# Kernel tuning notes

Hardware: AMD Instinct MI355X
Metric: run time of the kernel (lower is better)

Reference implementation:

```python
import jax, jax.numpy as jnp
from jax import lax
import numpy as np

B, CIN, COUT, WDIM, SIN, K = 8, 512, 512, 512, 64, 3
UP, DOWN, TAPS = 2, 2, 12
PX0, PX1, PY0, PY1 = 9, 8, 9, 8  # from StyleGAN3 padding formula for these rates
CLAMP, SLOPE = 256.0, 0.2
GAIN = float(np.sqrt(2.0))
FS_TMP, CUTOFF, HALFW = 128.0, 16.0, 16.0
DN = ('NCHW', 'OIHW', 'NCHW')


def _kaiser_beta(a):
    if a > 50.0:
        return 0.1102 * (a - 8.7)
    if a > 21.0:
        return 0.5842 * (a - 21.0) ** 0.4 + 0.07886 * (a - 21.0)
    return 0.0


def _firwin(numtaps, cutoff, width, fs):
    # replicates scipy.signal.firwin(numtaps, cutoff, width=width, fs=fs)
    nyq = fs / 2.0
    atten = 2.285 * (numtaps - 1) * np.pi * (width / nyq) + 7.95
    beta = _kaiser_beta(atten)
    win = np.kaiser(numtaps, beta)
    m = np.arange(numtaps) - (numtaps - 1) / 2.0
    fc = cutoff / nyq
    h = fc * np.sinc(fc * m) * win
    h /= h.sum()
    return h.astype(np.float32)


def setup_inputs() -> dict:
    key = jax.random.key(0)
    ks = jax.random.split(key, 4)
    f = jnp.asarray(_firwin(TAPS, CUTOFF, 2.0 * HALFW, FS_TMP))
    return {
        'x': jax.random.normal(ks[0], (B, CIN, SIN, SIN), jnp.float32),
        'w': jax.random.normal(ks[1], (B, WDIM), jnp.float32),
        'affine_w': jax.random.normal(ks[2], (CIN, WDIM), jnp.float32),
        'affine_b': jnp.ones((CIN,), jnp.float32),  # bias_init=1
        'conv_w': jax.random.normal(ks[3], (COUT, CIN, K, K), jnp.float32),
        'conv_b': jnp.zeros((COUT,), jnp.float32),
        'up_filter': f,
        'down_filter': f,  # same cutoff/width/fs for in and out here
    }


def _depthwise(x, f1d, axis, stride=1, pad=(0, 0), lhs_dil=1):
    # separable depthwise FIR along one spatial axis (axis 2 = H, 3 = W)
    C, t = x.shape[1], f1d.shape[0]
    if axis == 2:
        k = jnp.broadcast_to(f1d.reshape(1, 1, t, 1), (C, 1, t, 1))
        return lax.conv_general_dilated(x, k, (stride, 1), [pad, (0, 0)],
                                        lhs_dilation=(lhs_dil, 1),
                                        feature_group_count=C, dimension_numbers=DN)
    k = jnp.broadcast_to(f1d.reshape(1, 1, 1, t), (C, 1, 1, t))
    return lax.conv_general_dilated(x, k, (1, stride), [(0, 0), pad],
                                    lhs_dilation=(1, lhs_dil),
                                    feature_group_count=C, dimension_numbers=DN)


def reference(x, w, affine_w, affine_b, conv_w, conv_b, up_filter, down_filter):
    # --- affine: FullyConnectedLayer(w_dim, in_channels, bias_init=1) ---
    styles = w @ (affine_w.T * (1.0 / np.sqrt(WDIM))) + affine_b  # [B, CIN]
    # --- modulated_conv2d with demodulation (input_gain = ema.rsqrt() = 1) ---
    wt = conv_w * lax.rsqrt(jnp.mean(conv_w ** 2, axis=(1, 2, 3), keepdims=True))
    s = styles * lax.rsqrt(jnp.mean(styles ** 2))
    ww = wt[None] * s[:, None, :, None, None]                     # [B,COUT,CIN,K,K]
    ww = ww * lax.rsqrt(jnp.sum(ww ** 2, axis=(2, 3, 4)) + 1e-8)[:, :, None, None, None]
    conv1 = lambda xi, wi: lax.conv_general_dilated(
        xi[None], wi, (1, 1), [(K - 1, K - 1)] * 2, dimension_numbers=DN)[0]
    x = jax.vmap(conv1)(x, ww)                                    # [B,COUT,66,66]
    # --- filtered_lrelu: bias -> upfirdn(up) -> lrelu*gain, clamp -> upfirdn(down) ---
    x = x + conv_b[None, :, None, None]
    fu = up_filter[::-1] * UP  # flip_filter=False; per-pass gain = up (total up^2)
    x = _depthwise(x, fu, 2, pad=(PY0, PY1 + UP - 1), lhs_dil=UP)
    x = _depthwise(x, fu, 3, pad=(PX0, PX1 + UP - 1), lhs_dil=UP)  # [B,COUT,138,138]
    x = jnp.clip(jnp.where(x >= 0, x, SLOPE * x) * GAIN, -CLAMP, CLAMP)
    fd = down_filter[::-1]
    x = _depthwise(x, fd, 2, stride=DOWN)
    x = _depthwise(x, fd, 3, stride=DOWN)                          # [B,COUT,64,64]
    return x
```

## Files before the change

### kernel.cpp

```cpp
#include <hip/hip_runtime.h>

typedef __attribute__((ext_vector_type(4))) float floatx4;
typedef __attribute__((ext_vector_type(8))) short short8;

#define AS1(p) ((const __attribute__((address_space(1))) unsigned int*)(p))
#define AS3(p) ((__attribute__((address_space(3))) unsigned int*)(p))

static __device__ __forceinline__ void async16(const void* g, void* l) {
  __builtin_amdgcn_global_load_lds(AS1(g), AS3(l), 16, 0, 0);
}

static __device__ __forceinline__ unsigned short f2bf(float f) {
  unsigned u = __float_as_uint(f);
  unsigned r = u + 0x7FFFu + ((u >> 16) & 1u);
  return (unsigned short)(r >> 16);
}
static __device__ __forceinline__ unsigned packbf(float lo, float hi) {
  unsigned ul = __float_as_uint(lo), uh = __float_as_uint(hi);
  ul = ul + 0x7FFFu + ((ul >> 16) & 1u);
  uh = uh + 0x7FFFu + ((uh >> 16) & 1u);
  return (ul >> 16) | (uh & 0xFFFF0000u);
}
static __device__ __forceinline__ float bf2f(unsigned short h) {
  return __uint_as_float(((unsigned)h) << 16);
}
static __device__ __forceinline__ float bf_lo(unsigned u) { return __uint_as_float(u << 16); }
static __device__ __forceinline__ float bf_hi(unsigned u) { return __uint_as_float(u & 0xFFFF0000u); }

__global__ void k_styles(const float* __restrict__ w, const float* __restrict__ aw,
                         const float* __restrict__ ab, float* __restrict__ styles) {
  int t = blockIdx.x * 256 + threadIdx.x;
  int b = t >> 9, c = t & 511;
  float acc = 0.f;
  for (int d = 0; d < 512; ++d) acc += w[b * 512 + d] * aw[c * 512 + d];
  styles[t] = acc * 0.04419417382415922f + ab[c];
}

__global__ void k_msr(const float* __restrict__ styles, float* __restrict__ msr) {
  __shared__ float red[256];
  float acc = 0.f;
  for (int i = threadIdx.x; i < 4096; i += 256) { float v = styles[i]; acc += v * v; }
  red[threadIdx.x] = acc; __syncthreads();
  for (int s = 128; s > 0; s >>= 1) {
    if ((int)threadIdx.x < s) red[threadIdx.x] += red[threadIdx.x + s];
    __syncthreads();
  }
  if (threadIdx.x == 0) *msr = rsqrtf(red[0] / 4096.0f);
}

__global__ void k_wstat(const float* __restrict__ cw, float* __restrict__ t, float* __restrict__ q) {
  int o = blockIdx.x, tid = threadIdx.x;
  __shared__ float red[256];
  float tot = 0.f;
  for (int i = tid; i < 512; i += 256) {
    const float* p = cw + ((size_t)o * 512 + i) * 9;
    float s = 0.f;
#pragma unroll
    for (int k = 0; k < 9; ++k) s += p[k] * p[k];
    q[o * 512 + i] = s;
    tot += s;
  }
  red[tid] = tot; __syncthreads();
  for (int s2 = 128; s2 > 0; s2 >>= 1) {
    if (tid < s2) red[tid] += red[tid + s2];
    __syncthreads();
  }
  if (tid == 0) t[o] = rsqrtf(red[0] / 4608.0f);
}

__global__ void k_dmod(const float* __restrict__ styles, const float* __restrict__ msr,
                       const float* __restrict__ t, const float* __restrict__ q,
                       float* __restrict__ g) {
  int idx = blockIdx.x * 256 + threadIdx.x;
  int b = idx >> 9, o = idx & 511;
  float m = *msr;
  float acc = 0.f;
  for (int i = 0; i < 512; ++i) {
    float s = styles[b * 512 + i] * m;
    acc += s * s * q[o * 512 + i];
  }
  float to = t[o];
  g[idx] = to * rsqrtf(to * to * acc + 1e-8f);
}

__global__ __launch_bounds__(256) void k_wpack(const float* __restrict__ cw,
                                               const float* __restrict__ styles,
                                               const float* __restrict__ msr,
                                               const float* __restrict__ g,
                                               unsigned short* __restrict__ wbf2) {
  __shared__ float raw[512][11];
  int o = blockIdx.x, tid = threadIdx.x;
  for (int i = tid; i < 512; i += 256) {
    const float* p = cw + ((size_t)o * 512 + i) * 9;
#pragma unroll
    for (int k = 0; k < 9; ++k) raw[i][k] = p[k];
  }
  __syncthreads();
  float m = *msr;
  const int nb = o >> 7, wn = (o >> 6) & 1, ni = (o >> 4) & 3, ol = o & 15;
  for (int b = 0; b < 8; ++b) {
    float gg = g[b * 512 + o];
    const size_t base_bo = ((size_t)(b * 4 + nb) * 2 + wn);
    for (int f = tid; f < 9 * 512; f += 256) {
      int s = f >> 9, i = f & 511;
      int ic = i >> 5, qq = (i >> 3) & 3, j = i & 7;
      float v = raw[i][s] * gg * (styles[b * 512 + i] * m);
      size_t idx = ((((base_bo * 9 + s) * 16 + ic) * 4 + ni) * 512) + (qq * 16 + ol) * 8 + j;
      wbf2[idx] = f2bf(v);
    }
  }
}

__global__ __launch_bounds__(256) void k_xpack(const float* __restrict__ x,
                                               unsigned short* __restrict__ xp) {
  __shared__ float tile[64][65];
  int Y = blockIdx.x, cc0 = blockIdx.y * 64, b = blockIdx.z;
  int tid = threadIdx.x;
  int yy = Y - 2;
  bool valid = (yy >= 0 && yy < 64);
  if (valid) {
    for (int it = 0; it < 16; ++it) {
      int f = it * 256 + tid;
      int cc = f >> 6, xx = f & 63;
      tile[xx][cc] = x[(((size_t)b * 512 + cc0 + cc) * 64 + yy) * 64 + xx];
    }
  }
  __syncthreads();
  for (int it = 0; it < 17; ++it) {
    int f = it * 256 + tid;
    int X = f >> 6, cc = f & 63;
    int xx = X - 2;
    float v = (valid && xx >= 0 && xx < 64) ? tile[xx][cc] : 0.f;
    xp[(((size_t)b * 68 + Y) * 68 + X) * 512 + cc0 + cc] = f2bf(v);
  }
}

__global__ __launch_bounds__(256, 2) void k_conv(const unsigned short* __restrict__ xp,
                                                 const unsigned short* __restrict__ wbf2,
                                                 const float* __restrict__ cb,
                                                 float* __restrict__ y) {
  __shared__ __align__(16) unsigned short lds[24576];
  const int tid = threadIdx.x;
  const int w = tid >> 6, lane = tid & 63;
  const int wm = w & 1, wn = w >> 1;
  const int q = lane >> 4, ln = lane & 15;

  const int xcd = blockIdx.x & 7;
  const int slot = blockIdx.x >> 3;
  const int combo = xcd * 4 + slot / 35;
  const int mt = slot % 35;
  const int nt = combo & 3;
  const int b = combo >> 2;
  const int m0 = mt * 128, n0 = nt * 128;
  const int oy0 = m0 / 66;

  const unsigned short* xpb = xp + (size_t)b * (68 * 68 * 512);

  size_t gof_p[6];
#pragma unroll
  for (int i = 0; i < 6; ++i) {
    int pv = w * 96 + i * 16 + (lane >> 2);
    int pve = pv < 339 ? pv : 339;
    int r = pve / 68, px = pve - r * 68;
    int Y = oy0 + r; if (Y > 67) Y = 67;
    int ch = ((lane & 3) ^ ((pve >> 1) & 3)) * 8;
    gof_p[i] = (size_t)(Y * 68 + px) * 512 + ch;
  }

  int pvA[4];
#pragma unroll
  for (int mi = 0; mi < 4; ++mi) {
    int p = m0 + wm * 64 + mi * 16 + ln; if (p > 4355) p = 4355;
    int oy = p / 66, ox = p - oy * 66;
    pvA[mi] = (oy - oy0) * 68 + ox;
  }

  const unsigned short* wB = wbf2 + (((size_t)(b * 4 + nt) * 2 + wn) * 294912) + (size_t)lane * 8;

  floatx4 acc[4][4];
#pragma unroll
  for (int i = 0; i < 4; ++i)
#pragma unroll
    for (int j = 0; j < 4; ++j) acc[i][j] = (floatx4){0.f, 0.f, 0.f, 0.f};

  unsigned short* pat0 = lds;
  unsigned short* pat1 = lds + 12288;

#pragma unroll
  for (int i = 0; i < 6; ++i)
    async16(xpb + gof_p[i], pat0 + (w * 96 + i * 16) * 32);

  short8 bF[4];
#pragma unroll
  for (int ni = 0; ni < 4; ++ni)
    bF[ni] = *(const short8*)(wB + ni * 512);

  for (int ic = 0; ic < 16; ++ic) {
    asm volatile("s_waitcnt vmcnt(0)" ::: "memory");
    asm volatile("s_barrier" ::: "memory");
    const unsigned short* pb = (ic & 1) ? pat1 : pat0;
    unsigned short* pn = (ic & 1) ? pat0 : pat1;
    const size_t pchan = (size_t)(ic + 1) * 32;
#pragma unroll
    for (int s = 0; s < 9; ++s) {
      if (s >= 1 && s <= 6 && ic < 15)
        async16(xpb + gof_p[s - 1] + pchan, pn + (w * 96 + (s - 1) * 16) * 32);
      const int sn = (s < 8) ? s + 1 : 0;
      const int icn = (s < 8) ? ic : (ic < 15 ? ic + 1 : 15);
      const unsigned short* wBn = wB + ((size_t)sn * 16 + icn) * 2048;
      short8 bN[4];
#pragma unroll
      for (int ni = 0; ni < 4; ++ni) bN[ni] = *(const short8*)(wBn + ni * 512);
      const int d = (s / 3) * 68 + (s % 3);
      short8 aF[4];
#pragma unroll
      for (int mi = 0; mi < 4; ++mi) {
        int pv = pvA[mi] + d;
        int off = pv * 32 + ((q ^ ((pv >> 1) & 3)) << 3);
        aF[mi] = *(const short8*)(pb + off);
      }
#pragma unroll
      for (int mi = 0; mi < 4; ++mi)
#pragma unroll
        for (int ni = 0; ni < 4; ++ni)
          acc[mi][ni] = __builtin_amdgcn_mfma_f32_16x16x32_bf16(aF[mi], bF[ni], acc[mi][ni], 0, 0, 0);
#pragma unroll
      for (int ni = 0; ni < 4; ++ni) bF[ni] = bN[ni];
    }
  }

  __syncthreads();
  float* slab = (float*)lds + w * 2176;
  const int pbase = m0 + wm * 64;
  const bool pok = (pbase + ln * 4) < 4356;
  float cbv[4];
#pragma unroll
  for (int ni = 0; ni < 4; ++ni) cbv[ni] = cb[n0 + wn * 64 + ni * 16 + ln];

#pragma unroll
  for (int pass = 0; pass < 2; ++pass) {
#pragma unroll
    for (int ni2 = 0; ni2 < 2; ++ni2) {
      const int ni = pass * 2 + ni2;
#pragma unroll
      for (int mi = 0; mi < 4; ++mi) {
        float4 v;
        v.x = acc[mi][ni][0] + cbv[ni];
        v.y = acc[mi][ni][1] + cbv[ni];
        v.z = acc[mi][ni][2] + cbv[ni];
        v.w = acc[mi][ni][3] + cbv[ni];
        *(float4*)&slab[(ni2 * 16 + ln) * 68 + mi * 16 + q * 4] = v;
      }
    }
#pragma unroll
    for (int i = 0; i < 8; ++i) {
      const int orow = i * 4 + q;
      const int o = n0 + wn * 64 + pass * 32 + orow;
      if (pok) {
        float4 vv = *(const float4*)&slab[orow * 68 + ln * 4];
        *(float4*)&y[((size_t)b * 512 + o) * 4356 + pbase + ln * 4] = vv;
      }
    }
  }
}

__global__ __launch_bounds__(256, 4) void k_updown(const float* __restrict__ yg,
                                                   const float* __restrict__ uf,
                                                   const float* __restrict__ df,
                                                   float* __restrict__ out) {
  __shared__ __align__(16) unsigned short zraw[138 * 88];
  __shared__ __align__(16) unsigned short t1buf[138 * 56];
  const int tid = threadIdx.x;
  const int plane = blockIdx.x >> 1;
  const int s = blockIdx.x & 1;
  const float* yp = yg + (size_t)plane * 4356;

  float fub[12], fuc[12], fdw[12];
#pragma unroll
  for (int i = 0; i < 12; ++i) {
    float u = uf[11 - i] * 2.0f;
    fub[i] = u;
    fuc[i] = u * 1.41421356237309515f;
    fdw[i] = df[11 - i];
  }

  float* ybuf = (float*)zraw;
  const int xoff = 32 * s - 4;
  for (int t = tid; t < 75 * 48; t += 256) {
    int row = t / 48, col = t - row * 48;
    int r = row - 4, x = xoff + col;
    float v = (r >= 0 && r < 66 && x >= 0 && x < 66) ? yp[r * 66 + x] : 0.f;
    ybuf[t] = v;
  }
  __syncthreads();

  for (int t = tid; t < 69 * 6; t += 256) {
    int v = t / 6, c = t - v * 6;
    float ae[8], ao[8];
#pragma unroll
    for (int e = 0; e < 8; ++e) { ae[e] = 0.f; ao[e] = 0.f; }
#pragma unroll
    for (int u = 0; u < 6; ++u) {
      const float* yr = &ybuf[(v + u) * 48 + 8 * c];
      float4 p0 = *(const float4*)yr;
      float4 p1 = *(const float4*)(yr + 4);
      float fe = fub[2 * u + 1], fo = fub[2 * u];
      ae[0] += p0.x * fe; ao[0] += p0.x * fo;
      ae[1] += p0.y * fe; ao[1] += p0.y * fo;
      ae[2] += p0.z * fe; ao[2] += p0.z * fo;
      ae[3] += p0.w * fe; ao[3] += p0.w * fo;
      ae[4] += p1.x * fe; ao[4] += p1.x * fo;
      ae[5] += p1.y * fe; ao[5] += p1.y * fo;
      ae[6] += p1.z * fe; ao[6] += p1.z * fo;
      ae[7] += p1.w * fe; ao[7] += p1.w * fo;
    }
    uint4 se, so;
    se.x = packbf(ae[0], ae[1]); se.y = packbf(ae[2], ae[3]);
    se.z = packbf(ae[4], ae[5]); se.w = packbf(ae[6], ae[7]);
    so.x = packbf(ao[0], ao[1]); so.y = packbf(ao[2], ao[3]);
    so.z = packbf(ao[4], ao[5]); so.w = packbf(ao[6], ao[7]);
    *(uint4*)&t1buf[(2 * v) * 56 + 8 * c] = se;
    *(uint4*)&t1buf[(2 * v + 1) * 56 + 8 * c] = so;
  }
  __syncthreads();

  for (int t = tid; t < 138 * 5; t += 256) {
    int Y = t / 5, k = t - Y * 5;
    const unsigned short* tr = &t1buf[Y * 56 + 8 * k];
    uint4 r0 = *(const uint4*)tr;
    uint4 r1 = *(const uint4*)(tr + 8);
    float a[14];
    a[0] = bf_lo(r0.x);  a[1] = bf_hi(r0.x);
    a[2] = bf_lo(r0.y);  a[3] = bf_hi(r0.y);
    a[4] = bf_lo(r0.z);  a[5] = bf_hi(r0.z);
    a[6] = bf_lo(r0.w);  a[7] = bf_hi(r0.w);
    a[8] = bf_lo(r1.x);  a[9] = bf_hi(r1.x);
    a[10] = bf_lo(r1.y); a[11] = bf_hi(r1.y);
    a[12] = bf_lo(r1.z); a[13] = bf_hi(r1.z);
    float ae[8], ao[8];
#pragma unroll
    for (int p = 0; p < 8; ++p) { ae[p] = 0.f; ao[p] = 0.f; }
#pragma unroll
    for (int u = 0; u < 6; ++u) {
      float fe = fuc[2 * u + 1], fo = fuc[2 * u];
#pragma unroll
      for (int p = 0; p < 8; ++p) {
        float tv = a[p + u];
        ae[p] += tv * fe;
        ao[p] += tv * fo;
      }
    }
    uint4 s0, s1;
    float ze[8], zo[8];
#pragma unroll
    for (int p = 0; p < 8; ++p) {
      float v0 = fmaxf(ae[p], 0.f) + 0.2f * fminf(ae[p], 0.f);
      float v1 = fmaxf(ao[p], 0.f) + 0.2f * fminf(ao[p], 0.f);
      ze[p] = fminf(fmaxf(v0, -256.f), 256.f);
      zo[p] = fminf(fmaxf(v1, -256.f), 256.f);
    }
    s0.x = packbf(ze[0], zo[0]); s0.y = packbf(ze[1], zo[1]);
    s0.z = packbf(ze[2], zo[2]); s0.w = packbf(ze[3], zo[3]);
    s1.x = packbf(ze[4], zo[4]); s1.y = packbf(ze[5], zo[5]);
    s1.z = packbf(ze[6], zo[6]); s1.w = packbf(ze[7], zo[7]);
    unsigned short* zr = &zraw[Y * 88 + 16 * k];
    *(uint4*)zr = s0;
    *(uint4*)(zr + 8) = s1;
  }
  __syncthreads();

  unsigned short* t2 = t1buf;
  for (int t = tid; t < 64 * 10; t += 256) {
    int yr = t / 10, k = t - yr * 10;
    float acc[8];
#pragma unroll
    for (int e = 0; e < 8; ++e) acc[e] = 0.f;
#pragma unroll
    for (int i = 0; i < 12; ++i) {
      uint4 zv = *(const uint4*)&zraw[(2 * yr + i) * 88 + 8 * k];
      float c = fdw[i];
      acc[0] += c * bf_lo(zv.x); acc[1] += c * bf_hi(zv.x);
      acc[2] += c * bf_lo(zv.y); acc[3] += c * bf_hi(zv.y);
      acc[4] += c * bf_lo(zv.z); acc[5] += c * bf_hi(zv.z);
      acc[6] += c * bf_lo(zv.w); acc[7] += c * bf_hi(zv.w);
    }
    uint4 st;
    st.x = packbf(acc[0], acc[1]); st.y = packbf(acc[2], acc[3]);
    st.z = packbf(acc[4], acc[5]); st.w = packbf(acc[6], acc[7]);
    *(uint4*)&t2[yr * 88 + 8 * k] = st;
  }
  __syncthreads();

  {
    int t = tid;
    int yr = t >> 2, ce = t & 3;
    const unsigned short* tr = &t2[yr * 88 + 16 * ce];
    uint4 q0 = *(const uint4*)tr;
    uint4 q1 = *(const uint4*)(tr + 8);
    uint4 q2 = *(const uint4*)(tr + 16);
    uint4 q3 = *(const uint4*)(tr + 24);
    float wv[26];
    wv[0] = bf_lo(q0.x);  wv[1] = bf_hi(q0.x);
    wv[2] = bf_lo(q0.y);  wv[3] = bf_hi(q0.y);
    wv[4] = bf_lo(q0.z);  wv[5] = bf_hi(q0.z);
    wv[6] = bf_lo(q0.w);  wv[7] = bf_hi(q0.w);
    wv[8] = bf_lo(q1.x);  wv[9] = bf_hi(q1.x);
    wv[10] = bf_lo(q1.y); wv[11] = bf_hi(q1.y);
    wv[12] = bf_lo(q1.z); wv[13] = bf_hi(q1.z);
    wv[14] = bf_lo(q1.w); wv[15] = bf_hi(q1.w);
    wv[16] = bf_lo(q2.x); wv[17] = bf_hi(q2.x);
    wv[18] = bf_lo(q2.y); wv[19] = bf_hi(q2.y);
    wv[20] = bf_lo(q2.z); wv[21] = bf_hi(q2.z);
    wv[22] = bf_lo(q2.w); wv[23] = bf_hi(q2.w);
    wv[24] = bf_lo(q3.x); wv[25] = bf_hi(q3.x);
    float ov[8];
#pragma unroll
    for (int e = 0; e < 8; ++e) {
      float acc = 0.f;
#pragma unroll
      for (int j = 0; j < 12; ++j) acc += fdw[j] * wv[2 * e + j];
      ov[e] = acc;
    }
    float* op = out + (size_t)plane * 4096 + yr * 64 + 32 * s + 8 * ce;
    *(float4*)op = (float4){ov[0], ov[1], ov[2], ov[3]};
    *(float4*)(op + 4) = (float4){ov[4], ov[5], ov[6], ov[7]};
  }
}

extern "C" void kernel_launch(void* const* d_in, const int* in_sizes, int n_in,
                              void* d_out, int out_size, void* d_ws, size_t ws_size,
                              hipStream_t stream) {
  const float* x  = (const float*)d_in[0];
  const float* w  = (const float*)d_in[1];
  const float* aw = (const float*)d_in[2];
  const float* ab = (const float*)d_in[3];
  const float* cw = (const float*)d_in[4];
  const float* cb = (const float*)d_in[5];
  const float* uf = (const float*)d_in[6];
  const float* df = (const float*)d_in[7];
  float* out = (float*)d_out;
  char* ws = (char*)d_ws;

  float* styles = (float*)(ws + 0);
  float* msr    = (float*)(ws + 16384);
  float* tbuf   = (float*)(ws + 16640);
  float* qbuf   = (float*)(ws + 18688);
  float* gbuf   = (float*)(ws + 1067264);
  unsigned short* xp   = (unsigned short*)(ws + 1083648);
  unsigned short* wbf2 = (unsigned short*)(ws + 38963456);
  float* yb            = (float*)(ws + 76712192);

  k_styles<<<16, 256, 0, stream>>>(w, aw, ab, styles);
  k_msr<<<1, 256, 0, stream>>>(styles, msr);
  k_wstat<<<512, 256, 0, stream>>>(cw, tbuf, qbuf);
  k_dmod<<<16, 256, 0, stream>>>(styles, msr, tbuf, qbuf, gbuf);
  k_wpack<<<512, 256, 0, stream>>>(cw, styles, msr, gbuf, wbf2);
  k_xpack<<<dim3(68, 8, 8), 256, 0, stream>>>(x, xp);
  k_conv<<<1120, 256, 0, stream>>>(xp, wbf2, cb, yb);
  k_updown<<<8192, 256, 0, stream>>>(yb, uf, df, out);
}
```

Baseline: 539.5 us.

## Halve conv M-tile, raise occupancy, deepen weight prefetch and simplify block mapping

The implicit-GEMM conv kernel's M tile shrinks from 128 to 64 output pixels, and its launch bound rises to 4 blocks per CU. The smaller LDS patch (4 rows padded to 80 columns) and fewer accumulators allow more blocks per CU and more blocks overall. Weight fragments are now prefetched two steps ahead with a partial vmcnt wait instead of a full drain. The XCD-aware block remap is dropped for a plain batch-interleaved mapping, and the output store is reorganised. Each block now reloads a larger halo relative to its work, and the change in L2 locality from the new block mapping is uncertain.

Measured after the change: 555.6 us. 1.03x slower.

```diff
diff --git a/kernel.cpp b/kernel.cpp
--- a/kernel.cpp
+++ b/kernel.cpp
@@ -135,104 +135,104 @@
   }
 }
 
-__global__ __launch_bounds__(256, 2) void k_conv(const unsigned short* __restrict__ xp,
+__global__ __launch_bounds__(256, 4) void k_conv(const unsigned short* __restrict__ xp,
                                                  const unsigned short* __restrict__ wbf2,
                                                  const float* __restrict__ cb,
                                                  float* __restrict__ y) {
-  __shared__ __align__(16) unsigned short lds[24576];
+  __shared__ __align__(16) unsigned short lds[20480];
   const int tid = threadIdx.x;
   const int w = tid >> 6, lane = tid & 63;
   const int wm = w & 1, wn = w >> 1;
   const int q = lane >> 4, ln = lane & 15;
 
-  const int xcd = blockIdx.x & 7;
-  const int slot = blockIdx.x >> 3;
-  const int combo = xcd * 4 + slot / 35;
-  const int mt = slot % 35;
-  const int nt = combo & 3;
-  const int b = combo >> 2;
-  const int m0 = mt * 128, n0 = nt * 128;
+  const int b = blockIdx.x & 7;
+  const int rest = blockIdx.x >> 3;
+  const int nt = rest / 69;
+  const int mt = rest - nt * 69;
+  const int m0 = mt * 64, n0 = nt * 128;
   const int oy0 = m0 / 66;
 
   const unsigned short* xpb = xp + (size_t)b * (68 * 68 * 512);
 
-  size_t gof_p[6];
-#pragma unroll
-  for (int i = 0; i < 6; ++i) {
-    int pv = w * 96 + i * 16 + (lane >> 2);
-    int pve = pv < 339 ? pv : 339;
-    int r = pve / 68, px = pve - r * 68;
-    int Y = oy0 + r; if (Y > 67) Y = 67;
-    int ch = ((lane & 3) ^ ((pve >> 1) & 3)) * 8;
-    gof_p[i] = (size_t)(Y * 68 + px) * 512 + ch;
-  }
-
-  int pvA[4];
-#pragma unroll
-  for (int mi = 0; mi < 4; ++mi) {
-    int p = m0 + wm * 64 + mi * 16 + ln; if (p > 4355) p = 4355;
+  size_t gof_p[5];
+  {
+    int Y = oy0 + w; if (Y > 67) Y = 67;
+#pragma unroll
+    for (int i = 0; i < 5; ++i) {
+      int col = i * 16 + (lane >> 2);
+      int vpad = w * 80 + col;
+      int X = col > 67 ? 67 : col;
+      int csrc = (lane & 3) ^ ((vpad >> 1) & 3);
+      gof_p[i] = (size_t)(Y * 68 + X) * 512 + csrc * 8;
+    }
+  }
+
+  int pvA[2];
+#pragma unroll
+  for (int mi = 0; mi < 2; ++mi) {
+    int p = m0 + wm * 32 + mi * 16 + ln; if (p > 4355) p = 4355;
     int oy = p / 66, ox = p - oy * 66;
-    pvA[mi] = (oy - oy0) * 68 + ox;
+    pvA[mi] = (oy - oy0) * 80 + ox;
   }
 
   const unsigned short* wB = wbf2 + (((size_t)(b * 4 + nt) * 2 + wn) * 294912) + (size_t)lane * 8;
 
-  floatx4 acc[4][4];
-#pragma unroll
-  for (int i = 0; i < 4; ++i)
+  floatx4 acc[2][4];
+#pragma unroll
+  for (int i = 0; i < 2; ++i)
 #pragma unroll
     for (int j = 0; j < 4; ++j) acc[i][j] = (floatx4){0.f, 0.f, 0.f, 0.f};
 
   unsigned short* pat0 = lds;
-  unsigned short* pat1 = lds + 12288;
-
-#pragma unroll
-  for (int i = 0; i < 6; ++i)
-    async16(xpb + gof_p[i], pat0 + (w * 96 + i * 16) * 32);
-
-  short8 bF[4];
-#pragma unroll
-  for (int ni = 0; ni < 4; ++ni)
-    bF[ni] = *(const short8*)(wB + ni * 512);
+  unsigned short* pat1 = lds + 10240;
+
+#pragma unroll
+  for (int i = 0; i < 5; ++i)
+    async16(xpb + gof_p[i], pat0 + (w * 80 + i * 16) * 32);
+
+  short8 bA[4], bB[4];
+#pragma unroll
+  for (int ni = 0; ni < 4; ++ni) bA[ni] = *(const short8*)(wB + ni * 512);
+#pragma unroll
+  for (int ni = 0; ni < 4; ++ni) bB[ni] = *(const short8*)(wB + 16 * 2048 + ni * 512);
 
   for (int ic = 0; ic < 16; ++ic) {
-    asm volatile("s_waitcnt vmcnt(0)" ::: "memory");
+    asm volatile("s_waitcnt vmcnt(8)" ::: "memory");
     asm volatile("s_barrier" ::: "memory");
     const unsigned short* pb = (ic & 1) ? pat1 : pat0;
     unsigned short* pn = (ic & 1) ? pat0 : pat1;
     const size_t pchan = (size_t)(ic + 1) * 32;
+    const int icn = ic < 15 ? ic + 1 : 15;
 #pragma unroll
     for (int s = 0; s < 9; ++s) {
-      if (s >= 1 && s <= 6 && ic < 15)
-        async16(xpb + gof_p[s - 1] + pchan, pn + (w * 96 + (s - 1) * 16) * 32);
-      const int sn = (s < 8) ? s + 1 : 0;
-      const int icn = (s < 8) ? ic : (ic < 15 ? ic + 1 : 15);
-      const unsigned short* wBn = wB + ((size_t)sn * 16 + icn) * 2048;
-      short8 bN[4];
-#pragma unroll
-      for (int ni = 0; ni < 4; ++ni) bN[ni] = *(const short8*)(wBn + ni * 512);
-      const int d = (s / 3) * 68 + (s % 3);
-      short8 aF[4];
-#pragma unroll
-      for (int mi = 0; mi < 4; ++mi) {
+      if (s < 5 && ic < 15)
+        async16(xpb + gof_p[s] + pchan, pn + (w * 80 + s * 16) * 32);
+      const int ss2 = (s <= 6) ? s + 2 : s - 7;
+      const int ic2 = (s <= 6) ? ic : icn;
+      const unsigned short* wBn = wB + ((size_t)(ss2 * 16 + ic2)) * 2048;
+      short8 bC[4];
+#pragma unroll
+      for (int ni = 0; ni < 4; ++ni) bC[ni] = *(const short8*)(wBn + ni * 512);
+      const int d = (s / 3) * 80 + (s % 3);
+      short8 aF[2];
+#pragma unroll
+      for (int mi = 0; mi < 2; ++mi) {
         int pv = pvA[mi] + d;
         int off = pv * 32 + ((q ^ ((pv >> 1) & 3)) << 3);
         aF[mi] = *(const short8*)(pb + off);
       }
 #pragma unroll
-      for (int mi = 0; mi < 4; ++mi)
+      for (int mi = 0; mi < 2; ++mi)
 #pragma unroll
         for (int ni = 0; ni < 4; ++ni)
-          acc[mi][ni] = __builtin_amdgcn_mfma_f32_16x16x32_bf16(aF[mi], bF[ni], acc[mi][ni], 0, 0, 0);
-#pragma unroll
-      for (int ni = 0; ni < 4; ++ni) bF[ni] = bN[ni];
-    }
-  }
-
-  __syncthreads();
-  float* slab = (float*)lds + w * 2176;
-  const int pbase = m0 + wm * 64;
-  const bool pok = (pbase + ln * 4) < 4356;
+          acc[mi][ni] = __builtin_amdgcn_mfma_f32_16x16x32_bf16(aF[mi], bA[ni], acc[mi][ni], 0, 0, 0);
+#pragma unroll
+      for (int ni = 0; ni < 4; ++ni) { bA[ni] = bB[ni]; bB[ni] = bC[ni]; }
+    }
+  }
+
+  float* slab = (float*)lds + w * 1152;
+  const int pbase = m0 + wm * 32;
   float cbv[4];
 #pragma unroll
   for (int ni = 0; ni < 4; ++ni) cbv[ni] = cb[n0 + wn * 64 + ni * 16 + ln];
@@ -243,23 +243,24 @@
     for (int ni2 = 0; ni2 < 2; ++ni2) {
       const int ni = pass * 2 + ni2;
 #pragma unroll
-      for (int mi = 0; mi < 4; ++mi) {
+      for (int mi = 0; mi < 2; ++mi) {
         float4 v;
         v.x = acc[mi][ni][0] + cbv[ni];
         v.y = acc[mi][ni][1] + cbv[ni];
         v.z = acc[mi][ni][2] + cbv[ni];
         v.w = acc[mi][ni][3] + cbv[ni];
-        *(float4*)&slab[(ni2 * 16 + ln) * 68 + mi * 16 + q * 4] = v;
+        *(float4*)&slab[(ni2 * 16 + ln) * 36 + mi * 16 + q * 4] = v;
       }
     }
-#pragma unroll
-    for (int i = 0; i < 8; ++i) {
-      const int orow = i * 4 + q;
-      const int o = n0 + wn * 64 + pass * 32 + orow;
-      if (pok) {
-        float4 vv = *(const float4*)&slab[orow * 68 + ln * 4];
-        *(float4*)&y[((size_t)b * 512 + o) * 4356 + pbase + ln * 4] = vv;
-      }
+    const int ol = lane >> 1;
+    const int ph = (lane & 1) * 16;
+    const int o = n0 + wn * 64 + pass * 32 + ol;
+    float* dst = &y[((size_t)b * 512 + o) * 4356 + pbase + ph];
+#pragma unroll
+    for (int j = 0; j < 4; ++j) {
+      const int p4 = pbase + ph + j * 4;
+      if (p4 < 4356)
+        *(float4*)(dst + j * 4) = *(const float4*)&slab[ol * 36 + ph + j * 4];
     }
   }
 }
@@ -456,6 +457,6 @@
   k_dmod<<<16, 256, 0, stream>>>(styles, msr, tbuf, qbuf, gbuf);
   k_wpack<<<512, 256, 0, stream>>>(cw, styles, msr, gbuf, wbf2);
   k_xpack<<<dim3(68, 8, 8), 256, 0, stream>>>(x, xp);
-  k_conv<<<1120, 256, 0, stream>>>(xp, wbf2, cb, yb);
+  k_conv<<<2208, 256, 0, stream>>>(xp, wbf2, cb, yb);
   k_updown<<<8192, 256, 0, stream>>>(yb, uf, df, out);
 }
```
